# Kernel tuning notes

Measured on AMD Instinct MI355X. Metric: run time of the kernel, lower is better.

## Reference

```python
import jax, jax.numpy as jnp
import numpy as np

D_HEAD = 64

def setup_inputs() -> dict:
    key = jax.random.key(0)
    k1, k2, k3, k4, k5 = jax.random.split(key, 5)
    b, s, d_model, n_heads, d_head = 2, 4096, 512, 8, D_HEAD
    x = jax.random.normal(k1, (b, s, d_model), dtype=jnp.float32)
    scale = 1.0 / np.sqrt(d_model)
    W_K = jax.random.normal(k2, (n_heads, d_head, d_model), dtype=jnp.float32) * scale
    W_Q = jax.random.normal(k3, (n_heads, d_head, d_model), dtype=jnp.float32) * scale
    W_V = jax.random.normal(k4, (n_heads, d_head, d_model), dtype=jnp.float32) * scale
    W_O = jax.random.normal(k5, (d_model, d_head * n_heads), dtype=jnp.float32) * scale
    return {"x": x, "W_K": W_K, "W_Q": W_Q, "W_V": W_V, "W_O": W_O}

def reference(x, W_K, W_Q, W_V, W_O):
    # x: [b, p, d]; W_{K,Q,V}: [i, h, d]; W_O: [d, i*h]
    s = x.shape[-2]
    k = jnp.einsum('ihd,bpd->biph', W_K, x)
    q = jnp.einsum('ihd,bpd->biph', W_Q, x)
    v = jnp.einsum('ihd,bpd->biph', W_V, x)
    scores = jnp.einsum('biph,biqh->biqp', k, q)  # [b, i, q, p]
    mask = jnp.tril(jnp.ones((s, s), dtype=scores.dtype))
    scores = jnp.tril(scores) - 1e10 * (1.0 - mask)
    attn = jax.nn.softmax(scores / np.sqrt(D_HEAD), axis=-1)
    z = jnp.einsum('biph,biqp->biqh', v, attn)  # [b, i, q, h]
    b, i, qlen, h = z.shape
    z_flat = jnp.transpose(z, (0, 2, 1, 3)).reshape(b, qlen, i * h)  # 'b i q h -> b q (i h)'
    out = jnp.einsum('df,bqf->bqd', W_O, z_flat)
    return out
```

## Files before the change

kernel.cpp:

```cpp
#include <hip/hip_runtime.h>
#include <hip/hip_bf16.h>


typedef __attribute__((ext_vector_type(4)))  float  f32x4;
typedef __attribute__((ext_vector_type(16))) float  f32x16;
typedef __attribute__((ext_vector_type(8)))  __bf16 bf16x8;
typedef __attribute__((ext_vector_type(8)))  unsigned short u16x8;
typedef __attribute__((ext_vector_type(4)))  unsigned int u32x4;

#define MFMA16(a, b, c) __builtin_amdgcn_mfma_f32_16x16x32_bf16((a), (b), (c), 0, 0, 0)
#define MFMA32(a, b, c) __builtin_amdgcn_mfma_f32_32x32x16_bf16((a), (b), (c), 0, 0, 0)
#define SWZ(g, r) ((g) ^ ((r) & 7))
#define SLOTS_BH 72

static __device__ __forceinline__ bf16x8 ld8(const __hip_bfloat16* p) {
    return *reinterpret_cast<const bf16x8*>(p);
}
static __device__ __forceinline__ __hip_bfloat16 tobf(float f) {
    return __float2bfloat16(f);
}
static __device__ __forceinline__ float exp2_raw(float x) {
    float r;
    asm("v_exp_f32 %0, %1" : "=v"(r) : "v"(x));
    return r;
}
static __device__ __forceinline__ unsigned cvt_pk(float lo, float hi) {
    unsigned r;
    asm("v_cvt_pk_bf16_f32 %0, %1, %2" : "=v"(r) : "v"(lo), "v"(hi));
    return r;
}
static __device__ __forceinline__ void pl32swap(unsigned& a, unsigned& b) {
    asm("v_permlane32_swap_b32 %0, %1" : "+v"(a), "+v"(b));
}
static __device__ __forceinline__ void gl_lds16(const __hip_bfloat16* g, __hip_bfloat16* l) {
    typedef __attribute__((address_space(1))) const unsigned int GU;
    typedef __attribute__((address_space(3))) unsigned int LU;
    __builtin_amdgcn_global_load_lds((GU*)(const void*)g, (LU*)(void*)l, 16, 0, 0);
}
static __device__ __forceinline__ int nchunks(int qi) { return (qi + 2) >> 1; }
static __device__ __forceinline__ int slot_off(int qi) {
    const int a = qi >> 1;
    return (qi & 1) ? (a + 1) * (a + 1) : a * a + a;
}

__global__ __launch_bounds__(256) void cast_all(
    const float* __restrict__ x,  const float* __restrict__ wk,
    const float* __restrict__ wq, const float* __restrict__ wv,
    const float* __restrict__ wo,
    __hip_bfloat16* __restrict__ xb,  __hip_bfloat16* __restrict__ wkb,
    __hip_bfloat16* __restrict__ wqb, __hip_bfloat16* __restrict__ wvb,
    __hip_bfloat16* __restrict__ wob)
{
    const int bid = blockIdx.x;
    const float* src;
    __hip_bfloat16* dst;
    int base;
    if (bid < 2048) { src = x; dst = xb; base = bid; }
    else {
        const int r = (bid - 2048) >> 7;
        base = (bid - 2048) & 127;
        src = (r == 0) ? wk : (r == 1) ? wq : (r == 2) ? wv : wo;
        dst = (r == 0) ? wkb : (r == 1) ? wqb : (r == 2) ? wvb : wob;
    }
    const size_t i = (size_t)base * 256 + threadIdx.x;
    const float4 a = *reinterpret_cast<const float4*>(src + i * 8);
    const float4 b = *reinterpret_cast<const float4*>(src + i * 8 + 4);
    u16x8 o;
    o[0] = __bfloat16_as_ushort(tobf(a.x));
    o[1] = __bfloat16_as_ushort(tobf(a.y));
    o[2] = __bfloat16_as_ushort(tobf(a.z));
    o[3] = __bfloat16_as_ushort(tobf(a.w));
    o[4] = __bfloat16_as_ushort(tobf(b.x));
    o[5] = __bfloat16_as_ushort(tobf(b.y));
    o[6] = __bfloat16_as_ushort(tobf(b.z));
    o[7] = __bfloat16_as_ushort(tobf(b.w));
    *reinterpret_cast<u16x8*>(dst + i * 8) = o;
}

__global__ __launch_bounds__(512) void qkv_gemm(
    const __hip_bfloat16* __restrict__ x,
    const __hip_bfloat16* __restrict__ Wk,
    const __hip_bfloat16* __restrict__ Wq,
    const __hip_bfloat16* __restrict__ Wv,
    __hip_bfloat16* __restrict__ Qo,
    __hip_bfloat16* __restrict__ Ko,
    __hip_bfloat16* __restrict__ Vt)
{
    __shared__ __hip_bfloat16 Xlds[2][128][64];
    __shared__ __hip_bfloat16 Wlds[2][128][64];

    const int mt = blockIdx.x;
    const int ni = blockIdx.y;
    const int z  = ni >> 2;
    const int m0 = mt * 128;

    const __hip_bfloat16* Wz =
        (z == 0 ? Wk : (z == 1 ? Wq : Wv)) + (size_t)(ni & 3) * 128 * 512;

    const int tid  = threadIdx.x;
    const int w    = tid >> 6;
    const int lane = tid & 63;
    const int q31  = lane & 31;
    const int hi   = lane >> 5;
    const int wm   = w >> 1;
    const int wn   = w & 1;

    const int r0l = w * 8 + (lane >> 3);
    const int cg  = (lane & 7) ^ (r0l & 7);
    const __hip_bfloat16* Xsrc = x  + (size_t)(m0 + r0l) * 512 + cg * 8;
    const __hip_bfloat16* Wsrc = Wz + (size_t)r0l * 512 + cg * 8;

    auto stage = [&](int buf, int k0) {
        gl_lds16(Xsrc + k0,                    &Xlds[buf][w * 8][0]);
        gl_lds16(Xsrc + k0 + (size_t)64 * 512, &Xlds[buf][w * 8 + 64][0]);
        gl_lds16(Wsrc + k0,                    &Wlds[buf][w * 8][0]);
        gl_lds16(Wsrc + k0 + (size_t)64 * 512, &Wlds[buf][w * 8 + 64][0]);
    };

    const int ra  = wm * 32 + q31;
    const int rb0 = wn * 64 + q31;
    const int rb1 = wn * 64 + 32 + q31;
    int gA[4], gB0[4], gB1[4];
#pragma unroll
    for (int ks = 0; ks < 4; ++ks) {
        gA[ks]  = SWZ(2 * ks + hi, ra)  * 8;
        gB0[ks] = SWZ(2 * ks + hi, rb0) * 8;
        gB1[ks] = SWZ(2 * ks + hi, rb1) * 8;
    }

    f32x16 ac0 = {}, ac1 = {};
    stage(0, 0);

    for (int it = 0; it < 8; ++it) {
        const int buf = it & 1;
        asm volatile("s_waitcnt vmcnt(0)" ::: "memory");
        __syncthreads();
        if (it < 7) stage(buf ^ 1, (it + 1) * 64);

        const __hip_bfloat16* xa  = &Xlds[buf][ra][0];
        const __hip_bfloat16* wb0 = &Wlds[buf][rb0][0];
        const __hip_bfloat16* wb1 = &Wlds[buf][rb1][0];

        __builtin_amdgcn_s_setprio(1);
#pragma unroll
        for (int ks = 0; ks < 4; ++ks) {
            bf16x8 a  = *(const bf16x8*)(xa  + gA[ks]);
            bf16x8 b0 = *(const bf16x8*)(wb0 + gB0[ks]);
            bf16x8 b1 = *(const bf16x8*)(wb1 + gB1[ks]);
            ac0 = MFMA32(a, b0, ac0);
            ac1 = MFMA32(a, b1, ac1);
        }
        __builtin_amdgcn_s_setprio(0);
    }

    const int b     = m0 >> 12;
    const int sbase = (m0 & 4095) + wm * 32;
    const int hc0   = (ni & 3) * 128 + wn * 64;

    if (z == 2) {
        auto vstore = [&](const f32x16& ac, int cf) {
            const int hcol = hc0 + cf * 32 + q31;
            const int h = hcol >> 6, dh = hcol & 63;
            __hip_bfloat16* vbase =
                Vt + ((size_t)(b * 8 + h) * 64 + dh) * 4096;
#pragma unroll
            for (int q2 = 0; q2 < 4; ++q2) {
                ushort4 pk;
                pk.x = __bfloat16_as_ushort(tobf(ac[q2 * 4 + 0]));
                pk.y = __bfloat16_as_ushort(tobf(ac[q2 * 4 + 1]));
                pk.z = __bfloat16_as_ushort(tobf(ac[q2 * 4 + 2]));
                pk.w = __bfloat16_as_ushort(tobf(ac[q2 * 4 + 3]));
                *reinterpret_cast<ushort4*>(vbase + sbase + 8 * q2 + 4 * hi) = pk;
            }
        };
        vstore(ac0, 0);
        vstore(ac1, 1);
    } else {
        const float scale = (z == 1) ? 0.18033688f : 1.0f;
        __hip_bfloat16* O = (z == 0) ? Ko : Qo;
        auto kstore = [&](const f32x16& ac, int cf) {
            const int hcol = hc0 + cf * 32 + q31;
            const int h = hcol >> 6, dh = hcol & 63;
            __hip_bfloat16* obase =
                O + (size_t)(b * 8 + h) * 4096 * 64 + dh;
#pragma unroll
            for (int reg = 0; reg < 16; ++reg) {
                const int srow = sbase + (reg & 3) + 8 * (reg >> 2) + 4 * hi;
                obase[(size_t)srow * 64] = tobf(ac[reg] * scale);
            }
        };
        kstore(ac0, 0);
        kstore(ac1, 1);
    }
}

__global__ __launch_bounds__(512) void attn_part(
    const __hip_bfloat16* __restrict__ Q,
    const __hip_bfloat16* __restrict__ K,
    const __hip_bfloat16* __restrict__ Vt,
    __hip_bfloat16* __restrict__ Zp,
    float* __restrict__ ML,
    __hip_bfloat16* __restrict__ Z)
{
    __shared__ __hip_bfloat16 Klds[2][64][64];
    __shared__ __hip_bfloat16 Vlds[2][64][64];
    __shared__ float als[8][32];

    const int id = blockIdx.x;
    const int bh = ((id & 7) << 1) | ((id >> 3) & 1);
    int rem = id >> 4;
    int qi = 15;
    for (;;) { const int ncq = nchunks(qi); if (rem < ncq) break; rem -= ncq; --qi; }
    const int c  = rem;
    const int nc = nchunks(qi);

    const int w    = threadIdx.x >> 6;
    const int lane = threadIdx.x & 63;
    const int q31  = lane & 31;
    const int hi   = lane >> 5;

    const __hip_bfloat16* Qb = Q  + (size_t)bh * 4096 * 64;
    const __hip_bfloat16* Kb = K  + (size_t)bh * 4096 * 64;
    const __hip_bfloat16* Vb = Vt + (size_t)bh * 64 * 4096;

    const int wbase = qi * 256 + w * 32;
    const int qrow  = wbase + q31;
    const int wqmax = wbase + 31;

    bf16x8 qf[4];
#pragma unroll
    for (int ks = 0; ks < 4; ++ks)
        qf[ks] = ld8(Qb + (size_t)qrow * 64 + ks * 16 + hi * 8);

    f32x16 za0 = {}, za1 = {};
    float l_ln = 0.0f;

    const int t0   = c * 8;
    const int tend = min(t0 + 8, 4 * qi + 4);
    const int nt   = tend - t0;

    int gsx[4];
#pragma unroll
    for (int ks = 0; ks < 4; ++ks) gsx[ks] = SWZ(2 * ks + hi, q31) * 8;

    const int r0l = w * 8 + (lane >> 3);
    const int cg  = (lane & 7) ^ (r0l & 7);
    const __hip_bfloat16* Ksrc = Kb + (size_t)r0l * 64 + cg * 8;
    const __hip_bfloat16* Vsrc = Vb + (size_t)r0l * 4096 + cg * 8;

    auto stage = [&](int buf, int t) {
        const int p0 = t * 64;
        gl_lds16(Ksrc + (size_t)p0 * 64, &Klds[buf][w * 8][0]);
        gl_lds16(Vsrc + p0,              &Vlds[buf][w * 8][0]);
    };

    stage(0, t0);

    for (int it = 0; it < nt; ++it) {
        const int t   = t0 + it;
        const int buf = it & 1;

        asm volatile("s_waitcnt vmcnt(0)" ::: "memory");
        __syncthreads();
        if (it + 1 < nt) stage(buf ^ 1, t + 1);

        const int p0 = t * 64;
        if (p0 > wqmax) continue;

        const __hip_bfloat16* kb0 = &Klds[buf][q31][0];
        const __hip_bfloat16* kb1 = &Klds[buf][32 + q31][0];

        f32x16 sa0 = {}, sa1 = {};
        __builtin_amdgcn_s_setprio(1);
#pragma unroll
        for (int ks = 0; ks < 4; ++ks) {
            bf16x8 k0 = *(const bf16x8*)(kb0 + gsx[ks]);
            bf16x8 k1 = *(const bf16x8*)(kb1 + gsx[ks]);
            sa0 = MFMA32(k0, qf[ks], sa0);
            sa1 = MFMA32(k1, qf[ks], sa1);
        }
        __builtin_amdgcn_s_setprio(0);

        if (p0 + 63 > wbase) {
#pragma unroll
            for (int reg = 0; reg < 16; ++reg) {
                const int pl = (reg & 3) + 8 * (reg >> 2) + 4 * hi;
                const int p  = p0 + pl;
                sa0[reg] = (p      <= qrow) ? sa0[reg] : -1.0e30f;
                sa1[reg] = (p + 32 <= qrow) ? sa1[reg] : -1.0e30f;
            }
        }

#pragma unroll
        for (int reg = 0; reg < 16; ++reg) {
            sa0[reg] = exp2_raw(sa0[reg]);
            sa1[reg] = exp2_raw(sa1[reg]);
        }

        float ts[8];
#pragma unroll
        for (int i = 0; i < 8; ++i)
            ts[i] = (sa0[i] + sa0[i + 8]) + (sa1[i] + sa1[i + 8]);
#pragma unroll
        for (int s = 4; s; s >>= 1)
#pragma unroll
            for (int i = 0; i < s; ++i) ts[i] += ts[i + s];
        l_ln += ts[0];

        bf16x8 pfrag[4];
#pragma unroll
        for (int kb = 0; kb < 4; ++kb) {
            const int e = (kb & 1) * 8;
            unsigned px, py, pu, pv;
            if (kb < 2) {
                px = cvt_pk(sa0[e + 0], sa0[e + 1]);
                py = cvt_pk(sa0[e + 2], sa0[e + 3]);
                pu = cvt_pk(sa0[e + 4], sa0[e + 5]);
                pv = cvt_pk(sa0[e + 6], sa0[e + 7]);
            } else {
                px = cvt_pk(sa1[e + 0], sa1[e + 1]);
                py = cvt_pk(sa1[e + 2], sa1[e + 3]);
                pu = cvt_pk(sa1[e + 4], sa1[e + 5]);
                pv = cvt_pk(sa1[e + 6], sa1[e + 7]);
            }
            pl32swap(px, pu);
            pl32swap(py, pv);
            u32x4 fw;
            fw[0] = px; fw[1] = py; fw[2] = pu; fw[3] = pv;
            pfrag[kb] = __builtin_bit_cast(bf16x8, fw);
        }

        const __hip_bfloat16* vb0 = &Vlds[buf][q31][0];
        const __hip_bfloat16* vb1 = &Vlds[buf][32 + q31][0];

        __builtin_amdgcn_s_setprio(1);
#pragma unroll
        for (int kb = 0; kb < 4; ++kb) {
            bf16x8 v0 = *(const bf16x8*)(vb0 + gsx[kb]);
            bf16x8 v1 = *(const bf16x8*)(vb1 + gsx[kb]);
            za0 = MFMA32(pfrag[kb], v0, za0);
            za1 = MFMA32(pfrag[kb], v1, za1);
        }
        __builtin_amdgcn_s_setprio(0);
    }

    float lt = l_ln + __shfl_xor(l_ln, 32);

    if (nc == 1) {
        if (hi == 0) als[w][q31] = 1.0f / lt;
        const int b = bh >> 3, h = bh & 7;
#pragma unroll
        for (int reg = 0; reg < 16; ++reg) {
            const int q = (reg & 3) + 8 * (reg >> 2) + 4 * hi;
            const float inv = als[w][q];
            __hip_bfloat16* zo =
                Z + ((size_t)b * 4096 + qi * 256 + w * 32 + q) * 512 + h * 64 + q31;
            zo[0]  = tobf(za0[reg] * inv);
            zo[32] = tobf(za1[reg] * inv);
        }
    } else {
        const int slot = bh * SLOTS_BH + slot_off(qi) + c;
        if (hi == 0)
            ML[(size_t)slot * 512 + 256 + w * 32 + q31] = lt;
#pragma unroll
        for (int reg = 0; reg < 16; ++reg) {
            const int q = (reg & 3) + 8 * (reg >> 2) + 4 * hi;
            const size_t base =
                (size_t)slot * 16384 + (size_t)(w * 32 + q) * 64 + q31;
            Zp[base]      = tobf(za0[reg]);
            Zp[base + 32] = tobf(za1[reg]);
        }
    }
}

__global__ __launch_bounds__(512) void attn_combine(
    const __hip_bfloat16* __restrict__ Zp,
    const float* __restrict__ ML,
    __hip_bfloat16* __restrict__ Z)
{
    const int qi = blockIdx.x + 2;
    const int bh = blockIdx.y;
    const int nc = nchunks(qi);
    const int q    = threadIdx.x >> 1;
    const int half = threadIdx.x & 1;

    const int slot0 = bh * SLOTS_BH + slot_off(qi);

    float L = 0.0f;
    float acc[32];
#pragma unroll
    for (int j = 0; j < 32; ++j) acc[j] = 0.0f;

    for (int i = 0; i < nc; ++i) {
        L += ML[(size_t)(slot0 + i) * 512 + 256 + q];
        const __hip_bfloat16* zp =
            Zp + (size_t)(slot0 + i) * 16384 + (size_t)q * 64 + half * 32;
#pragma unroll
        for (int v = 0; v < 4; ++v) {
            bf16x8 z = ld8(zp + v * 8);
#pragma unroll
            for (int j = 0; j < 8; ++j) acc[v * 8 + j] += (float)z[j];
        }
    }

    const float inv = 1.0f / L;
    const int b = bh >> 3, h = bh & 7;
    __hip_bfloat16* zo =
        Z + ((size_t)b * 4096 + qi * 256 + q) * 512 + h * 64 + half * 32;
#pragma unroll
    for (int v = 0; v < 4; ++v) {
        u16x8 o;
#pragma unroll
        for (int j = 0; j < 8; ++j)
            o[j] = __bfloat16_as_ushort(tobf(acc[v * 8 + j] * inv));
        *reinterpret_cast<u16x8*>(zo + v * 8) = o;
    }
}

__global__ __launch_bounds__(512) void out_gemm(
    const __hip_bfloat16* __restrict__ Zf,
    const __hip_bfloat16* __restrict__ Wo,
    float* __restrict__ out)
{
    __shared__ __hip_bfloat16 Alds[2][128][64];
    __shared__ __hip_bfloat16 Blds[2][128][64];

    const int mt = blockIdx.x;
    const int ni = blockIdx.y;
    const int m0 = mt * 128;
    const int n0 = ni * 128;

    const int tid  = threadIdx.x;
    const int w    = tid >> 6;
    const int lane = tid & 63;
    const int q31  = lane & 31;
    const int hi   = lane >> 5;
    const int wm   = w >> 1;
    const int wn   = w & 1;

    const int r0l = w * 8 + (lane >> 3);
    const int cg  = (lane & 7) ^ (r0l & 7);
    const __hip_bfloat16* Asrc = Zf + (size_t)(m0 + r0l) * 512 + cg * 8;
    const __hip_bfloat16* Bsrc = Wo + (size_t)(n0 + r0l) * 512 + cg * 8;

    auto stage = [&](int buf, int k0) {
        gl_lds16(Asrc + k0,                    &Alds[buf][w * 8][0]);
        gl_lds16(Asrc + k0 + (size_t)64 * 512, &Alds[buf][w * 8 + 64][0]);
        gl_lds16(Bsrc + k0,                    &Blds[buf][w * 8][0]);
        gl_lds16(Bsrc + k0 + (size_t)64 * 512, &Blds[buf][w * 8 + 64][0]);
    };

    const int ra  = wm * 32 + q31;
    const int rb0 = wn * 64 + q31;
    const int rb1 = wn * 64 + 32 + q31;
    int gA[4], gB0[4], gB1[4];
#pragma unroll
    for (int ks = 0; ks < 4; ++ks) {
        gA[ks]  = SWZ(2 * ks + hi, ra)  * 8;
        gB0[ks] = SWZ(2 * ks + hi, rb0) * 8;
        gB1[ks] = SWZ(2 * ks + hi, rb1) * 8;
    }

    f32x16 ac0 = {}, ac1 = {};
    stage(0, 0);

    for (int it = 0; it < 8; ++it) {
        const int buf = it & 1;
        asm volatile("s_waitcnt vmcnt(0)" ::: "memory");
        __syncthreads();
        if (it < 7) stage(buf ^ 1, (it + 1) * 64);

        const __hip_bfloat16* xa  = &Alds[buf][ra][0];
        const __hip_bfloat16* wb0 = &Blds[buf][rb0][0];
        const __hip_bfloat16* wb1 = &Blds[buf][rb1][0];

        __builtin_amdgcn_s_setprio(1);
#pragma unroll
        for (int ks = 0; ks < 4; ++ks) {
            bf16x8 a  = *(const bf16x8*)(xa  + gA[ks]);
            bf16x8 b0 = *(const bf16x8*)(wb0 + gB0[ks]);
            bf16x8 b1 = *(const bf16x8*)(wb1 + gB1[ks]);
            ac0 = MFMA32(a, b0, ac0);
            ac1 = MFMA32(a, b1, ac1);
        }
        __builtin_amdgcn_s_setprio(0);
    }

    const int row0 = m0 + wm * 32;
    const int col0 = n0 + wn * 64;
#pragma unroll
    for (int reg = 0; reg < 16; ++reg) {
        const int r = row0 + (reg & 3) + 8 * (reg >> 2) + 4 * hi;
        out[(size_t)r * 512 + col0 + q31]      = ac0[reg];
        out[(size_t)r * 512 + col0 + 32 + q31] = ac1[reg];
    }
}

extern "C" void kernel_launch(void* const* d_in, const int* in_sizes, int n_in,
                              void* d_out, int out_size, void* d_ws, size_t ws_size,
                              hipStream_t stream)
{
    const float* x_f  = (const float*)d_in[0];
    const float* Wk_f = (const float*)d_in[1];
    const float* Wq_f = (const float*)d_in[2];
    const float* Wv_f = (const float*)d_in[3];
    const float* Wo_f = (const float*)d_in[4];
    float* out = (float*)d_out;

    char* ws = (char*)d_ws;
    const size_t szQKV = (size_t)16 * 4096 * 64 * sizeof(__hip_bfloat16);
    const size_t szX   = (size_t)8192 * 512 * sizeof(__hip_bfloat16);
    const size_t szW   = (size_t)8 * 64 * 512 * sizeof(__hip_bfloat16);
    const size_t szZp  = (size_t)16 * SLOTS_BH * 256 * 64 * sizeof(__hip_bfloat16);
    const size_t szML  = (size_t)16 * SLOTS_BH * 512 * sizeof(float);

    size_t off = 0;
    __hip_bfloat16* Qb  = (__hip_bfloat16*)(ws + off); off += szQKV;
    __hip_bfloat16* Kb  = (__hip_bfloat16*)(ws + off); off += szQKV;
    __hip_bfloat16* Vt  = (__hip_bfloat16*)(ws + off); off += szQKV;
    __hip_bfloat16* Zb  = (__hip_bfloat16*)(ws + off); off += szX;
    __hip_bfloat16* Wob = (__hip_bfloat16*)(ws + off); off += szW;
    const size_t trans = off;
    __hip_bfloat16* xb  = (__hip_bfloat16*)(ws + trans);
    __hip_bfloat16* Wkb = (__hip_bfloat16*)(ws + trans + szX);
    __hip_bfloat16* Wqb = (__hip_bfloat16*)(ws + trans + szX + szW);
    __hip_bfloat16* Wvb = (__hip_bfloat16*)(ws + trans + szX + 2 * szW);
    __hip_bfloat16* Zp  = (__hip_bfloat16*)(ws + trans);
    float*          ML  = (float*)(ws + trans + szZp);

    cast_all<<<2048 + 4 * 128, 256, 0, stream>>>(
        x_f, Wk_f, Wq_f, Wv_f, Wo_f, xb, Wkb, Wqb, Wvb, Wob);

    qkv_gemm<<<dim3(64, 12),    512, 0, stream>>>(xb, Wkb, Wqb, Wvb, Qb, Kb, Vt);
    attn_part<<<dim3(1152),     512, 0, stream>>>(Qb, Kb, Vt, Zp, ML, Zb);
    attn_combine<<<dim3(14, 16), 512, 0, stream>>>(Zp, ML, Zb);
    out_gemm<<<dim3(64, 4),     512, 0, stream>>>(Zb, Wob, out);
}
```

Measured before the change: 101.5 us.

## Fuse fp32-to-bf16 cast of x into QKV GEMM staging

Removes the separate cast pass over x by having qkv_gemm load fp32 x directly into registers, convert to bf16, and write swizzled into LDS after the MFMA phase. The cast kernel now only converts weights, and the workspace layout is adjusted so Zp/ML no longer alias the dropped xb buffer. This saves writing and re-reading a bf16 copy of x, but the qkv GEMM now reads fp32 x once per N-tile (12 times), with register-staged loads instead of direct-to-LDS loads.

```diff
diff --git a/kernel.cpp b/kernel.cpp
--- a/kernel.cpp
+++ b/kernel.cpp
@@ -44,24 +44,17 @@
 }
 
 __global__ __launch_bounds__(256) void cast_all(
-    const float* __restrict__ x,  const float* __restrict__ wk,
-    const float* __restrict__ wq, const float* __restrict__ wv,
-    const float* __restrict__ wo,
-    __hip_bfloat16* __restrict__ xb,  __hip_bfloat16* __restrict__ wkb,
-    __hip_bfloat16* __restrict__ wqb, __hip_bfloat16* __restrict__ wvb,
-    __hip_bfloat16* __restrict__ wob)
+    const float* __restrict__ wk, const float* __restrict__ wq,
+    const float* __restrict__ wv, const float* __restrict__ wo,
+    __hip_bfloat16* __restrict__ wkb, __hip_bfloat16* __restrict__ wqb,
+    __hip_bfloat16* __restrict__ wvb, __hip_bfloat16* __restrict__ wob)
 {
     const int bid = blockIdx.x;
-    const float* src;
-    __hip_bfloat16* dst;
-    int base;
-    if (bid < 2048) { src = x; dst = xb; base = bid; }
-    else {
-        const int r = (bid - 2048) >> 7;
-        base = (bid - 2048) & 127;
-        src = (r == 0) ? wk : (r == 1) ? wq : (r == 2) ? wv : wo;
-        dst = (r == 0) ? wkb : (r == 1) ? wqb : (r == 2) ? wvb : wob;
-    }
+    const int r   = bid >> 7;
+    const int base = bid & 127;
+    const float* src = (r == 0) ? wk : (r == 1) ? wq : (r == 2) ? wv : wo;
+    __hip_bfloat16* dst = (r == 0) ? wkb : (r == 1) ? wqb : (r == 2) ? wvb : wob;
+
     const size_t i = (size_t)base * 256 + threadIdx.x;
     const float4 a = *reinterpret_cast<const float4*>(src + i * 8);
     const float4 b = *reinterpret_cast<const float4*>(src + i * 8 + 4);
@@ -78,7 +71,7 @@
 }
 
 __global__ __launch_bounds__(512) void qkv_gemm(
-    const __hip_bfloat16* __restrict__ x,
+    const float* __restrict__ x,
     const __hip_bfloat16* __restrict__ Wk,
     const __hip_bfloat16* __restrict__ Wq,
     const __hip_bfloat16* __restrict__ Wv,
@@ -105,16 +98,28 @@
     const int wm   = w >> 1;
     const int wn   = w & 1;
 
-    const int r0l = w * 8 + (lane >> 3);
-    const int cg  = (lane & 7) ^ (r0l & 7);
-    const __hip_bfloat16* Xsrc = x  + (size_t)(m0 + r0l) * 512 + cg * 8;
-    const __hip_bfloat16* Wsrc = Wz + (size_t)r0l * 512 + cg * 8;
-
-    auto stage = [&](int buf, int k0) {
-        gl_lds16(Xsrc + k0,                    &Xlds[buf][w * 8][0]);
-        gl_lds16(Xsrc + k0 + (size_t)64 * 512, &Xlds[buf][w * 8 + 64][0]);
+    const int g   = lane & 7;
+    const int r0  = w * 8 + (lane >> 3);
+    const int xslot = SWZ(g, r0) * 8;
+    const float* Xs0 = x + (size_t)(m0 + r0) * 512 + g * 8;
+    const float* Xs1 = Xs0 + (size_t)64 * 512;
+
+    const int cg = g ^ (r0 & 7);
+    const __hip_bfloat16* Wsrc = Wz + (size_t)r0 * 512 + cg * 8;
+
+    auto stageW = [&](int buf, int k0) {
         gl_lds16(Wsrc + k0,                    &Wlds[buf][w * 8][0]);
         gl_lds16(Wsrc + k0 + (size_t)64 * 512, &Wlds[buf][w * 8 + 64][0]);
+    };
+    auto writeX = [&](int buf, const float4& a0, const float4& a1,
+                               const float4& b0, const float4& b1) {
+        u32x4 wa, wb;
+        wa[0] = cvt_pk(a0.x, a0.y); wa[1] = cvt_pk(a0.z, a0.w);
+        wa[2] = cvt_pk(a1.x, a1.y); wa[3] = cvt_pk(a1.z, a1.w);
+        wb[0] = cvt_pk(b0.x, b0.y); wb[1] = cvt_pk(b0.z, b0.w);
+        wb[2] = cvt_pk(b1.x, b1.y); wb[3] = cvt_pk(b1.z, b1.w);
+        *(u32x4*)&Xlds[buf][r0][xslot]      = wa;
+        *(u32x4*)&Xlds[buf][r0 + 64][xslot] = wb;
     };
 
     const int ra  = wm * 32 + q31;
@@ -129,13 +134,30 @@
     }
 
     f32x16 ac0 = {}, ac1 = {};
-    stage(0, 0);
+
+    {
+        float4 a0 = *(const float4*)(Xs0);
+        float4 a1 = *(const float4*)(Xs0 + 4);
+        float4 b0 = *(const float4*)(Xs1);
+        float4 b1 = *(const float4*)(Xs1 + 4);
+        writeX(0, a0, a1, b0, b1);
+        stageW(0, 0);
+    }
 
     for (int it = 0; it < 8; ++it) {
         const int buf = it & 1;
         asm volatile("s_waitcnt vmcnt(0)" ::: "memory");
         __syncthreads();
-        if (it < 7) stage(buf ^ 1, (it + 1) * 64);
+
+        float4 a0, a1, b0, b1;
+        if (it < 7) {
+            const int k1 = (it + 1) * 64;
+            a0 = *(const float4*)(Xs0 + k1);
+            a1 = *(const float4*)(Xs0 + k1 + 4);
+            b0 = *(const float4*)(Xs1 + k1);
+            b1 = *(const float4*)(Xs1 + k1 + 4);
+            stageW(buf ^ 1, k1);
+        }
 
         const __hip_bfloat16* xa  = &Xlds[buf][ra][0];
         const __hip_bfloat16* wb0 = &Wlds[buf][rb0][0];
@@ -145,12 +167,14 @@
 #pragma unroll
         for (int ks = 0; ks < 4; ++ks) {
             bf16x8 a  = *(const bf16x8*)(xa  + gA[ks]);
-            bf16x8 b0 = *(const bf16x8*)(wb0 + gB0[ks]);
-            bf16x8 b1 = *(const bf16x8*)(wb1 + gB1[ks]);
-            ac0 = MFMA32(a, b0, ac0);
-            ac1 = MFMA32(a, b1, ac1);
+            bf16x8 bb0 = *(const bf16x8*)(wb0 + gB0[ks]);
+            bf16x8 bb1 = *(const bf16x8*)(wb1 + gB1[ks]);
+            ac0 = MFMA32(a, bb0, ac0);
+            ac1 = MFMA32(a, bb1, ac1);
         }
         __builtin_amdgcn_s_setprio(0);
+
+        if (it < 7) writeX(buf ^ 1, a0, a1, b0, b1);
     }
 
     const int b     = m0 >> 12;
@@ -521,17 +545,16 @@
     __hip_bfloat16* Zb  = (__hip_bfloat16*)(ws + off); off += szX;
     __hip_bfloat16* Wob = (__hip_bfloat16*)(ws + off); off += szW;
     const size_t trans = off;
-    __hip_bfloat16* xb  = (__hip_bfloat16*)(ws + trans);
-    __hip_bfloat16* Wkb = (__hip_bfloat16*)(ws + trans + szX);
-    __hip_bfloat16* Wqb = (__hip_bfloat16*)(ws + trans + szX + szW);
-    __hip_bfloat16* Wvb = (__hip_bfloat16*)(ws + trans + szX + 2 * szW);
-    __hip_bfloat16* Zp  = (__hip_bfloat16*)(ws + trans);
-    float*          ML  = (float*)(ws + trans + szZp);
-
-    cast_all<<<2048 + 4 * 128, 256, 0, stream>>>(
-        x_f, Wk_f, Wq_f, Wv_f, Wo_f, xb, Wkb, Wqb, Wvb, Wob);
-
-    qkv_gemm<<<dim3(64, 12),    512, 0, stream>>>(xb, Wkb, Wqb, Wvb, Qb, Kb, Vt);
+    __hip_bfloat16* Wkb = (__hip_bfloat16*)(ws + trans);
+    __hip_bfloat16* Wqb = (__hip_bfloat16*)(ws + trans + szW);
+    __hip_bfloat16* Wvb = (__hip_bfloat16*)(ws + trans + 2 * szW);
+    __hip_bfloat16* Zp  = (__hip_bfloat16*)(ws + trans + 3 * szW);
+    float*          ML  = (float*)(ws + trans + 3 * szW + szZp);
+
+    cast_all<<<512, 256, 0, stream>>>(
+        Wk_f, Wq_f, Wv_f, Wo_f, Wkb, Wqb, Wvb, Wob);
+
+    qkv_gemm<<<dim3(64, 12),    512, 0, stream>>>(x_f, Wkb, Wqb, Wvb, Qb, Kb, Vt);
     attn_part<<<dim3(1152),     512, 0, stream>>>(Qb, Kb, Vt, Zp, ML, Zb);
     attn_combine<<<dim3(14, 16), 512, 0, stream>>>(Zp, ML, Zb);
     out_gemm<<<dim3(64, 4),     512, 0, stream>>>(Zb, Wob, out);
```

After: 103.4 us. Within noise of the previous version (+1.9%).
